# Performance work log

Measured on AMD Instinct MI355X. Metric: run time of the kernel, lower is better.

The kernel has to match this reference:

```python
import jax, jax.numpy as jnp
import numpy as np

ALPHA = 5.0
LAMBDA = 1.0


def setup_inputs() -> dict:
    key = jax.random.key(0)
    k1, k2 = jax.random.split(key)
    N, BITS, NCLASS = 2048, 64, 32
    b = jax.random.normal(k1, (N, BITS), dtype=jnp.float32)
    y = jax.random.randint(k2, (N,), 0, NCLASS, dtype=jnp.int32)
    return {"b": b, "y": y}


def reference(b, y):
    # similarity = 0.5 * <b_i, b_j>  -> [N, N]
    sim = 0.5 * (b @ b.T)
    # affinity: same-label pairs (equivalent to onehot(y) @ onehot(y).T > 0)
    aff = y[:, None] == y[None, :]  # [N, N] bool
    N = sim.shape[0]

    def step(carry, i):
        loss_sum, cnt = carry
        pos = aff[i]            # [N] bool, positives for row i
        theta = sim[i]          # [N]
        # triple[p, n] = theta_pos[p] - theta_neg[n] - alpha, clamped
        t = jnp.clip(theta[:, None] - theta[None, :] - ALPHA, -100.0, 50.0)
        # -(t - log(1 + exp(t))) == log1p(exp(t)) - t  (== softplus(-t))
        val = jnp.log1p(jnp.exp(t)) - t
        mask = pos[:, None] & (~pos)[None, :]
        npairs = mask.sum()
        valid = pos.any() & (~pos).any()
        row_loss = jnp.where(
            valid,
            jnp.where(mask, val, 0.0).sum() / jnp.maximum(npairs, 1).astype(val.dtype),
            0.0,
        )
        return (loss_sum + row_loss, cnt + valid.astype(jnp.float32)), None

    init = (jnp.float32(0.0), jnp.float32(0.0))
    (loss_sum, cnt), _ = jax.lax.scan(step, init, jnp.arange(N))
    loss1 = jnp.where(cnt > 0, loss_sum / jnp.maximum(cnt, 1.0), 0.0)
    # quantization loss (sign has zero gradient, same as torch)
    loss2 = jnp.mean((b - jnp.sign(b)) ** 2)
    total = loss1 + LAMBDA * loss2
    return total, loss1, loss2
```

## Files before the change

kernel.cpp:

```cpp
#include <hip/hip_runtime.h>
#include <math.h>

#define NROW 2048
#define BITS 64
#define MB 1024
#define RPB 8
#define JQ 2
#define NBLK (NROW / RPB)
#define NWV (MB / 64)
#define MAXPOS 256
#define MAXP2 (MAXPOS / 2)

#define LN2_F   0.6931471805599453f
#define THSCALE 0.7213475204444817f
#define A_SC    7.213475204444817f

__global__ __launch_bounds__(256) void bt_kernel(const float* __restrict__ b,
                                                 float* __restrict__ bT)
{
    __shared__ float tile[64][65];
    const int t  = threadIdx.x;
    const int j0 = blockIdx.x * 64;
    {
        const int jj = t >> 2, q = t & 3;
        const float4* b4 = reinterpret_cast<const float4*>(b + (size_t)(j0 + jj) * BITS);
#pragma unroll
        for (int m = 0; m < 4; ++m) {
            const float4 v = b4[q * 4 + m];
            const int col = q * 16 + m * 4;
            tile[jj][col + 0] = v.x; tile[jj][col + 1] = v.y;
            tile[jj][col + 2] = v.z; tile[jj][col + 3] = v.w;
        }
    }
    __syncthreads();
    {
        const int k = t >> 2, q = t & 3;
#pragma unroll
        for (int s = 0; s < 4; ++s) {
            float4 v;
            v.x = tile[q * 16 + s * 4 + 0][k];
            v.y = tile[q * 16 + s * 4 + 1][k];
            v.z = tile[q * 16 + s * 4 + 2][k];
            v.w = tile[q * 16 + s * 4 + 3][k];
            *reinterpret_cast<float4*>(&bT[(size_t)k * NROW + j0 + q * 16 + s * 4]) = v;
        }
    }
}

template <bool TR>
__global__ __launch_bounds__(MB) void dhn_main(
    const float* __restrict__ b, const float* __restrict__ bT,
    const int* __restrict__ y,
    float* __restrict__ blockLoss, float* __restrict__ blockValid,
    float* __restrict__ blockQ)
{
    const int br  = blockIdx.x;
    const int i0  = br * RPB;
    const int tid = threadIdx.x;
    const int w = tid >> 6, lane = tid & 63;

    __shared__ __align__(16) float  biT[BITS * RPB];
    __shared__ __align__(16) float  posPe[RPB][MAXPOS + 8];
    __shared__ __align__(16) float2 posSM[RPB][MAXP2 + 4];
    __shared__ int   waveTot[RPB][NWV];
    __shared__ int   waveBase[RPB][NWV];
    __shared__ int   pcnt[RPB];
    __shared__ float wred[NWV], wq[NWV];

    if (tid < BITS * RPB) {
        const int k = tid >> 3, r = tid & 7;
        biT[tid] = b[(size_t)(i0 + r) * BITS + k];
    }
    __syncthreads();

    float th[JQ][RPB] = {};
    if constexpr (TR) {
        const float2* bt2 = reinterpret_cast<const float2*>(bT);
        const float4* bi4 = reinterpret_cast<const float4*>(biT);
#pragma unroll 8
        for (int k = 0; k < BITS; ++k) {
            const float2 bj = bt2[k * (NROW / 2) + tid];
            const float4 bA = bi4[k * 2 + 0];
            const float4 bB = bi4[k * 2 + 1];
            th[0][0] += bj.x * bA.x; th[0][1] += bj.x * bA.y;
            th[0][2] += bj.x * bA.z; th[0][3] += bj.x * bA.w;
            th[0][4] += bj.x * bB.x; th[0][5] += bj.x * bB.y;
            th[0][6] += bj.x * bB.z; th[0][7] += bj.x * bB.w;
            th[1][0] += bj.y * bA.x; th[1][1] += bj.y * bA.y;
            th[1][2] += bj.y * bA.z; th[1][3] += bj.y * bA.w;
            th[1][4] += bj.y * bB.x; th[1][5] += bj.y * bB.y;
            th[1][6] += bj.y * bB.z; th[1][7] += bj.y * bB.w;
        }
    } else {
        for (int k = 0; k < BITS; ++k) {
#pragma unroll
            for (int q = 0; q < JQ; ++q) {
                const float v = b[(size_t)(JQ * tid + q) * BITS + k];
#pragma unroll
                for (int r = 0; r < RPB; ++r) th[q][r] += v * biT[k * RPB + r];
            }
        }
    }

    const int2 y2 = reinterpret_cast<const int2*>(y)[tid];
    const int yj[JQ] = { y2.x, y2.y };
    int yr[RPB];
#pragma unroll
    for (int r = 0; r < RPB; ++r) yr[r] = y[i0 + r];

    float ev[JQ][RPB];
    int pm[RPB], cnt[RPB];
#pragma unroll
    for (int r = 0; r < RPB; ++r) {
        int m = 0;
#pragma unroll
        for (int q = 0; q < JQ; ++q) {
            const float t2 = th[q][r] * THSCALE;
            const bool f = (yj[q] == yr[r]);
            ev[q][r] = __builtin_amdgcn_exp2f(f ? -t2 : t2 + A_SC);
            if (f) m |= 1 << q;
        }
        pm[r] = m;
        cnt[r] = __popc(m);
    }

    int excl[RPB];
#pragma unroll
    for (int r = 0; r < RPB; ++r) {
        int v = cnt[r];
#pragma unroll
        for (int off = 1; off < 64; off <<= 1) {
            const int t2 = __shfl_up(v, off);
            if (lane >= off) v += t2;
        }
        excl[r] = v - cnt[r];
        if (lane == 63) waveTot[r][w] = v;
    }
    __syncthreads();
    if (tid < RPB) {
        int base = 0;
#pragma unroll
        for (int wv = 0; wv < NWV; ++wv) { waveBase[tid][wv] = base; base += waveTot[tid][wv]; }
        pcnt[tid] = base;
    }
    __syncthreads();

#pragma unroll
    for (int r = 0; r < RPB; ++r) {
        int o = waveBase[r][w] + excl[r];
#pragma unroll
        for (int q = 0; q < JQ; ++q) {
            if ((pm[r] >> q) & 1) {
                if (o < MAXPOS) posPe[r][o] = ev[q][r];
                ++o;
            }
        }
    }
    if (tid < RPB * 8) {
        const int r = tid >> 3, q = tid & 7;
        const int P = pcnt[r] < MAXPOS ? pcnt[r] : MAXPOS;
        const int idx = P + q;
        if (idx < ((P + 7) & ~7)) posPe[r][idx] = 0.f;
    }
    __syncthreads();

    {
        const int r  = tid >> 7;
        const int pp = tid & 127;
        const int P  = pcnt[r] < MAXPOS ? pcnt[r] : MAXPOS;
        const int P2pad = ((P + 7) & ~7) >> 1;
        if (pp < P2pad) {
            const float p0 = posPe[r][2 * pp + 0];
            const float p1 = posPe[r][2 * pp + 1];
            posSM[r][pp] = make_float2(p0 + p1, p0 * p1);
        }
    }
    __syncthreads();

    float total = 0.f;
#pragma unroll
    for (int r = 0; r < RPB; ++r) {
        const int Pc = pcnt[r];
        const int P  = Pc < MAXPOS ? Pc : MAXPOS;
        const int PG = (((P + 7) & ~7) >> 1) >> 2;
        const float e0  = (pm[r] & 1) ? 0.f : ev[0][r];
        const float e1  = (pm[r] & 2) ? 0.f : ev[1][r];
        const float e20 = e0 * e0;
        const float e21 = e1 * e1;
        float a0 = 0.f, a1 = 0.f;
        const float4* sm4 = reinterpret_cast<const float4*>(&posSM[r][0]);
        for (int g = 0; g < PG; ++g) {
            const float4 A = sm4[2 * g + 0];
            const float4 B = sm4[2 * g + 1];
            a0 += __builtin_amdgcn_logf(fmaf(e20, A.y, fmaf(e0, A.x, 1.f)))
                + __builtin_amdgcn_logf(fmaf(e20, A.w, fmaf(e0, A.z, 1.f)))
                + __builtin_amdgcn_logf(fmaf(e20, B.y, fmaf(e0, B.x, 1.f)))
                + __builtin_amdgcn_logf(fmaf(e20, B.w, fmaf(e0, B.z, 1.f)));
            a1 += __builtin_amdgcn_logf(fmaf(e21, A.y, fmaf(e1, A.x, 1.f)))
                + __builtin_amdgcn_logf(fmaf(e21, A.w, fmaf(e1, A.z, 1.f)))
                + __builtin_amdgcn_logf(fmaf(e21, B.y, fmaf(e1, B.x, 1.f)))
                + __builtin_amdgcn_logf(fmaf(e21, B.w, fmaf(e1, B.z, 1.f)));
        }
        const bool valid = (Pc > 0) && (Pc < NROW);
        const float denom = (float)Pc * (float)(NROW - Pc);
        total += valid ? (a0 + a1) / denom : 0.f;
    }
    total *= LN2_F;

    float q2 = 0.f;
    if (tid < BITS * RPB) {
        const float x  = biT[tid];
        const float sg = (x > 0.f) ? 1.f : ((x < 0.f) ? -1.f : 0.f);
        const float d  = x - sg;
        q2 = d * d;
    }

#pragma unroll
    for (int off = 32; off > 0; off >>= 1) {
        total += __shfl_xor(total, off);
        q2    += __shfl_xor(q2, off);
    }
    if (lane == 0) { wred[w] = total; wq[w] = q2; }
    __syncthreads();
    if (tid == 0) {
        float tl = 0.f, tq = 0.f;
#pragma unroll
        for (int v = 0; v < NWV; ++v) { tl += wred[v]; tq += wq[v]; }
        blockLoss[br] = tl;
        blockQ[br]    = tq;
        float vc = 0.f;
#pragma unroll
        for (int r = 0; r < RPB; ++r)
            vc += ((pcnt[r] > 0) && (pcnt[r] < NROW)) ? 1.f : 0.f;
        blockValid[br] = vc;
    }
}

__global__ __launch_bounds__(256) void dhn_final_kernel(
    const float* __restrict__ blockLoss, const float* __restrict__ blockValid,
    const float* __restrict__ blockQ, float* __restrict__ out)
{
    const int tid = threadIdx.x;
    const int w = tid >> 6, lane = tid & 63;
    __shared__ float r1[4], r2[4], r3[4];

    float sl = 0.f, sv = 0.f, sq = 0.f;
    for (int i = tid; i < NBLK; i += 256) {
        sl += blockLoss[i]; sv += blockValid[i]; sq += blockQ[i];
    }
#pragma unroll
    for (int off = 32; off > 0; off >>= 1) {
        sl += __shfl_xor(sl, off);
        sv += __shfl_xor(sv, off);
        sq += __shfl_xor(sq, off);
    }
    if (lane == 0) { r1[w] = sl; r2[w] = sv; r3[w] = sq; }
    __syncthreads();
    if (tid == 0) {
        float SL = 0.f, SV = 0.f, SQ = 0.f;
#pragma unroll
        for (int v = 0; v < 4; ++v) { SL += r1[v]; SV += r2[v]; SQ += r3[v]; }
        const float loss1 = (SV > 0.f) ? SL / fmaxf(SV, 1.f) : 0.f;
        const float loss2 = SQ / (float)(NROW * BITS);
        out[0] = loss1 + 1.0f * loss2;
        out[1] = loss1;
        out[2] = loss2;
    }
}

extern "C" void kernel_launch(void* const* d_in, const int* in_sizes, int n_in,
                              void* d_out, int out_size, void* d_ws, size_t ws_size,
                              hipStream_t stream) {
    const float* b = (const float*)d_in[0];
    const int*   y = (const int*)d_in[1];
    float* out = (float*)d_out;

    float* blockLoss  = (float*)d_ws;
    float* blockValid = (float*)((char*)d_ws + 4096);
    float* blockQ     = (float*)((char*)d_ws + 8192);
    float* bT         = (float*)((char*)d_ws + 16384);

    const size_t need = 16384 + (size_t)BITS * NROW * sizeof(float);
    if (ws_size >= need) {
        bt_kernel<<<NROW / 64, 256, 0, stream>>>(b, bT);
        dhn_main<true><<<NBLK, MB, 0, stream>>>(b, bT, y, blockLoss, blockValid, blockQ);
    } else {
        dhn_main<false><<<NBLK, MB, 0, stream>>>(b, nullptr, y, blockLoss, blockValid, blockQ);
    }
    dhn_final_kernel<<<1, 256, 0, stream>>>(blockLoss, blockValid, blockQ, out);
}
```

Baseline: 45.90 us.

## Precompute positives by label bucketing and split columns across two blocks

Adds a prep kernel that builds a per-label histogram and an index list, plus a pos kernel that computes each row's positive exp terms directly from that list. The main kernel no longer needs block-wide prefix scans and compaction, and runs over a 2D grid so each 512-thread block handles half of the columns. The aim is to remove the heavy scan and sync phases and to raise parallelism. In exchange it adds two extra launches and global round trips, drops the fallback path when the workspace is too small, and lowers the positive cap to 128.

```diff
diff --git a/kernel.cpp b/kernel.cpp
--- a/kernel.cpp
+++ b/kernel.cpp
@@ -3,83 +3,152 @@
 
 #define NROW 2048
 #define BITS 64
-#define MB 1024
+#define MB 512
 #define RPB 8
 #define JQ 2
-#define NBLK (NROW / RPB)
-#define NWV (MB / 64)
-#define MAXPOS 256
-#define MAXP2 (MAXPOS / 2)
+#define NRG (NROW / RPB)
+#define NSL 2
+#define JSL (NROW / NSL)
+#define MAXPOS 128
 
 #define LN2_F   0.6931471805599453f
 #define THSCALE 0.7213475204444817f
 #define A_SC    7.213475204444817f
 
-__global__ __launch_bounds__(256) void bt_kernel(const float* __restrict__ b,
-                                                 float* __restrict__ bT)
-{
-    __shared__ float tile[64][65];
-    const int t  = threadIdx.x;
-    const int j0 = blockIdx.x * 64;
-    {
-        const int jj = t >> 2, q = t & 3;
-        const float4* b4 = reinterpret_cast<const float4*>(b + (size_t)(j0 + jj) * BITS);
-#pragma unroll
-        for (int m = 0; m < 4; ++m) {
-            const float4 v = b4[q * 4 + m];
-            const int col = q * 16 + m * 4;
-            tile[jj][col + 0] = v.x; tile[jj][col + 1] = v.y;
-            tile[jj][col + 2] = v.z; tile[jj][col + 3] = v.w;
-        }
-    }
-    __syncthreads();
-    {
-        const int k = t >> 2, q = t & 3;
-#pragma unroll
-        for (int s = 0; s < 4; ++s) {
-            float4 v;
-            v.x = tile[q * 16 + s * 4 + 0][k];
-            v.y = tile[q * 16 + s * 4 + 1][k];
-            v.z = tile[q * 16 + s * 4 + 2][k];
-            v.w = tile[q * 16 + s * 4 + 3][k];
-            *reinterpret_cast<float4*>(&bT[(size_t)k * NROW + j0 + q * 16 + s * 4]) = v;
-        }
-    }
-}
-
-template <bool TR>
+__global__ __launch_bounds__(256) void prep_kernel(
+    const float* __restrict__ b, const int* __restrict__ y,
+    float* __restrict__ bT, int* __restrict__ offG, int* __restrict__ idxG)
+{
+    union U {
+        float tile[64][65];
+        struct { int ys[NROW]; int hist[32]; int offL[33]; } s;
+    };
+    __shared__ U u;
+    const int t = threadIdx.x;
+
+    if (blockIdx.x < 32) {
+        const int j0 = blockIdx.x * 64;
+        {
+            const int jj = t >> 2, q = t & 3;
+            const float4* b4 = reinterpret_cast<const float4*>(b + (size_t)(j0 + jj) * BITS);
+#pragma unroll
+            for (int m = 0; m < 4; ++m) {
+                const float4 v = b4[q * 4 + m];
+                const int col = q * 16 + m * 4;
+                u.tile[jj][col + 0] = v.x; u.tile[jj][col + 1] = v.y;
+                u.tile[jj][col + 2] = v.z; u.tile[jj][col + 3] = v.w;
+            }
+        }
+        __syncthreads();
+        {
+            const int k = t >> 2, q = t & 3;
+#pragma unroll
+            for (int s = 0; s < 4; ++s) {
+                float4 v;
+                v.x = u.tile[q * 16 + s * 4 + 0][k];
+                v.y = u.tile[q * 16 + s * 4 + 1][k];
+                v.z = u.tile[q * 16 + s * 4 + 2][k];
+                v.w = u.tile[q * 16 + s * 4 + 3][k];
+                *reinterpret_cast<float4*>(&bT[(size_t)k * NROW + j0 + q * 16 + s * 4]) = v;
+            }
+        }
+        return;
+    }
+
+    for (int k = t; k < NROW; k += 256) u.s.ys[k] = y[k];
+    if (t < 32) u.s.hist[t] = 0;
+    __syncthreads();
+    for (int k = t; k < NROW; k += 256) atomicAdd(&u.s.hist[u.s.ys[k]], 1);
+    __syncthreads();
+    const int w = t >> 6, lane = t & 63;
+    if (w == 0) {
+        int v = (lane < 32) ? u.s.hist[lane] : 0;
+#pragma unroll
+        for (int off = 1; off < 32; off <<= 1) {
+            const int tv = __shfl_up(v, off);
+            if (lane >= off) v += tv;
+        }
+        if (lane < 32) { u.s.offL[lane + 1] = v; offG[lane + 1] = v; }
+        if (lane == 0) { u.s.offL[0] = 0; offG[0] = 0; }
+    }
+    __syncthreads();
+    const unsigned long long lm = (1ull << lane) - 1ull;
+    for (int s8 = 0; s8 < 8; ++s8) {
+        const int lab = w * 8 + s8;
+        int base = u.s.offL[lab];
+        for (int c = 0; c < NROW / 64; ++c) {
+            const int j = c * 64 + lane;
+            const bool f = (u.s.ys[j] == lab);
+            const unsigned long long mp = __ballot(f);
+            if (f) idxG[base + (int)__popcll(mp & lm)] = j;
+            base += (int)__popcll(mp);
+        }
+    }
+}
+
+__global__ __launch_bounds__(256) void pos_kernel(
+    const float* __restrict__ b, const int* __restrict__ y,
+    const int* __restrict__ offG, const int* __restrict__ idxG,
+    float* __restrict__ posPeG)
+{
+    __shared__ __align__(16) float biS[4][BITS];
+    const int t = threadIdx.x, w = t >> 6, lane = t & 63;
+    const int i = blockIdx.x * 4 + w;
+    if (lane < BITS) biS[w][lane] = b[(size_t)i * BITS + lane];
+    __syncthreads();
+    const int yi = y[i];
+    const int st = offG[yi];
+    const int P  = offG[yi + 1] - st;
+    const float4* bi4 = reinterpret_cast<const float4*>(&biS[w][0]);
+    for (int p = lane; p < MAXPOS; p += 64) {
+        float val = 0.f;
+        if (p < P) {
+            const int jp = idxG[st + p];
+            const float4* rp = reinterpret_cast<const float4*>(b + (size_t)jp * BITS);
+            float acc = 0.f;
+#pragma unroll
+            for (int k4 = 0; k4 < BITS / 4; ++k4) {
+                const float4 a = bi4[k4], v = rp[k4];
+                acc += a.x * v.x + a.y * v.y + a.z * v.z + a.w * v.w;
+            }
+            val = __builtin_amdgcn_exp2f(-THSCALE * acc);
+        }
+        posPeG[(size_t)i * MAXPOS + p] = val;
+    }
+}
+
 __global__ __launch_bounds__(MB) void dhn_main(
     const float* __restrict__ b, const float* __restrict__ bT,
-    const int* __restrict__ y,
-    float* __restrict__ blockLoss, float* __restrict__ blockValid,
-    float* __restrict__ blockQ)
-{
-    const int br  = blockIdx.x;
-    const int i0  = br * RPB;
-    const int tid = threadIdx.x;
+    const int* __restrict__ y, const int* __restrict__ offG,
+    const float* __restrict__ posPeG,
+    float* __restrict__ blockLoss, float* __restrict__ blockQ)
+{
+    const int rg    = blockIdx.x;
+    const int slice = blockIdx.y;
+    const int i0    = rg * RPB;
+    const int tid   = threadIdx.x;
     const int w = tid >> 6, lane = tid & 63;
 
     __shared__ __align__(16) float  biT[BITS * RPB];
-    __shared__ __align__(16) float  posPe[RPB][MAXPOS + 8];
-    __shared__ __align__(16) float2 posSM[RPB][MAXP2 + 4];
-    __shared__ int   waveTot[RPB][NWV];
-    __shared__ int   waveBase[RPB][NWV];
-    __shared__ int   pcnt[RPB];
-    __shared__ float wred[NWV], wq[NWV];
-
-    if (tid < BITS * RPB) {
-        const int k = tid >> 3, r = tid & 7;
-        biT[tid] = b[(size_t)(i0 + r) * BITS + k];
+    __shared__ __align__(16) float2 posSM[RPB][MAXPOS / 2];
+    __shared__ float wred[MB / 64], wq[MB / 64];
+
+    biT[tid] = b[(size_t)(i0 + (tid & 7)) * BITS + (tid >> 3)];
+    {
+        const float2 pg = reinterpret_cast<const float2*>(posPeG)
+                              [(size_t)(i0 + w) * (MAXPOS / 2) + lane];
+        posSM[w][lane] = make_float2(pg.x + pg.y, pg.x * pg.y);
     }
     __syncthreads();
 
     float th[JQ][RPB] = {};
-    if constexpr (TR) {
+    {
         const float2* bt2 = reinterpret_cast<const float2*>(bT);
         const float4* bi4 = reinterpret_cast<const float4*>(biT);
+        const int jb = slice * (JSL / 2) + tid;
 #pragma unroll 8
         for (int k = 0; k < BITS; ++k) {
-            const float2 bj = bt2[k * (NROW / 2) + tid];
+            const float2 bj = bt2[k * (NROW / 2) + jb];
             const float4 bA = bi4[k * 2 + 0];
             const float4 bB = bi4[k * 2 + 1];
             th[0][0] += bj.x * bA.x; th[0][1] += bj.x * bA.y;
@@ -91,124 +160,43 @@
             th[1][4] += bj.y * bB.x; th[1][5] += bj.y * bB.y;
             th[1][6] += bj.y * bB.z; th[1][7] += bj.y * bB.w;
         }
-    } else {
-        for (int k = 0; k < BITS; ++k) {
-#pragma unroll
-            for (int q = 0; q < JQ; ++q) {
-                const float v = b[(size_t)(JQ * tid + q) * BITS + k];
-#pragma unroll
-                for (int r = 0; r < RPB; ++r) th[q][r] += v * biT[k * RPB + r];
-            }
-        }
-    }
-
-    const int2 y2 = reinterpret_cast<const int2*>(y)[tid];
-    const int yj[JQ] = { y2.x, y2.y };
-    int yr[RPB];
-#pragma unroll
-    for (int r = 0; r < RPB; ++r) yr[r] = y[i0 + r];
-
-    float ev[JQ][RPB];
-    int pm[RPB], cnt[RPB];
+    }
+    const int2 y2 = reinterpret_cast<const int2*>(y)[slice * (JSL / 2) + tid];
+
+    float total = 0.f;
 #pragma unroll
     for (int r = 0; r < RPB; ++r) {
-        int m = 0;
-#pragma unroll
-        for (int q = 0; q < JQ; ++q) {
-            const float t2 = th[q][r] * THSCALE;
-            const bool f = (yj[q] == yr[r]);
-            ev[q][r] = __builtin_amdgcn_exp2f(f ? -t2 : t2 + A_SC);
-            if (f) m |= 1 << q;
-        }
-        pm[r] = m;
-        cnt[r] = __popc(m);
-    }
-
-    int excl[RPB];
-#pragma unroll
-    for (int r = 0; r < RPB; ++r) {
-        int v = cnt[r];
-#pragma unroll
-        for (int off = 1; off < 64; off <<= 1) {
-            const int t2 = __shfl_up(v, off);
-            if (lane >= off) v += t2;
-        }
-        excl[r] = v - cnt[r];
-        if (lane == 63) waveTot[r][w] = v;
-    }
-    __syncthreads();
-    if (tid < RPB) {
-        int base = 0;
-#pragma unroll
-        for (int wv = 0; wv < NWV; ++wv) { waveBase[tid][wv] = base; base += waveTot[tid][wv]; }
-        pcnt[tid] = base;
-    }
-    __syncthreads();
-
-#pragma unroll
-    for (int r = 0; r < RPB; ++r) {
-        int o = waveBase[r][w] + excl[r];
-#pragma unroll
-        for (int q = 0; q < JQ; ++q) {
-            if ((pm[r] >> q) & 1) {
-                if (o < MAXPOS) posPe[r][o] = ev[q][r];
-                ++o;
-            }
-        }
-    }
-    if (tid < RPB * 8) {
-        const int r = tid >> 3, q = tid & 7;
-        const int P = pcnt[r] < MAXPOS ? pcnt[r] : MAXPOS;
-        const int idx = P + q;
-        if (idx < ((P + 7) & ~7)) posPe[r][idx] = 0.f;
-    }
-    __syncthreads();
-
-    {
-        const int r  = tid >> 7;
-        const int pp = tid & 127;
-        const int P  = pcnt[r] < MAXPOS ? pcnt[r] : MAXPOS;
-        const int P2pad = ((P + 7) & ~7) >> 1;
-        if (pp < P2pad) {
-            const float p0 = posPe[r][2 * pp + 0];
-            const float p1 = posPe[r][2 * pp + 1];
-            posSM[r][pp] = make_float2(p0 + p1, p0 * p1);
-        }
-    }
-    __syncthreads();
-
-    float total = 0.f;
-#pragma unroll
-    for (int r = 0; r < RPB; ++r) {
-        const int Pc = pcnt[r];
-        const int P  = Pc < MAXPOS ? Pc : MAXPOS;
-        const int PG = (((P + 7) & ~7) >> 1) >> 2;
-        const float e0  = (pm[r] & 1) ? 0.f : ev[0][r];
-        const float e1  = (pm[r] & 2) ? 0.f : ev[1][r];
-        const float e20 = e0 * e0;
-        const float e21 = e1 * e1;
-        float a0 = 0.f, a1 = 0.f;
+        const int yr = y[i0 + r];
+        const int P  = offG[yr + 1] - offG[yr];
+        const int PG = ((P + 7) & ~7) >> 3;
+        const float x0 = __builtin_amdgcn_exp2f(th[0][r] * THSCALE + A_SC);
+        const float x1 = __builtin_amdgcn_exp2f(th[1][r] * THSCALE + A_SC);
+        const float e0 = (y2.x == yr) ? 0.f : x0;
+        const float e1 = (y2.y == yr) ? 0.f : x1;
+        const float e20 = e0 * e0, e21 = e1 * e1;
+        float la0 = 0.f, la1 = 0.f;
         const float4* sm4 = reinterpret_cast<const float4*>(&posSM[r][0]);
         for (int g = 0; g < PG; ++g) {
             const float4 A = sm4[2 * g + 0];
             const float4 B = sm4[2 * g + 1];
-            a0 += __builtin_amdgcn_logf(fmaf(e20, A.y, fmaf(e0, A.x, 1.f)))
-                + __builtin_amdgcn_logf(fmaf(e20, A.w, fmaf(e0, A.z, 1.f)))
-                + __builtin_amdgcn_logf(fmaf(e20, B.y, fmaf(e0, B.x, 1.f)))
-                + __builtin_amdgcn_logf(fmaf(e20, B.w, fmaf(e0, B.z, 1.f)));
-            a1 += __builtin_amdgcn_logf(fmaf(e21, A.y, fmaf(e1, A.x, 1.f)))
-                + __builtin_amdgcn_logf(fmaf(e21, A.w, fmaf(e1, A.z, 1.f)))
-                + __builtin_amdgcn_logf(fmaf(e21, B.y, fmaf(e1, B.x, 1.f)))
-                + __builtin_amdgcn_logf(fmaf(e21, B.w, fmaf(e1, B.z, 1.f)));
-        }
-        const bool valid = (Pc > 0) && (Pc < NROW);
-        const float denom = (float)Pc * (float)(NROW - Pc);
-        total += valid ? (a0 + a1) / denom : 0.f;
+            la0 += (__builtin_amdgcn_logf(fmaf(e20, A.y, fmaf(e0, A.x, 1.f)))
+                  + __builtin_amdgcn_logf(fmaf(e20, A.w, fmaf(e0, A.z, 1.f))))
+                 + (__builtin_amdgcn_logf(fmaf(e20, B.y, fmaf(e0, B.x, 1.f)))
+                  + __builtin_amdgcn_logf(fmaf(e20, B.w, fmaf(e0, B.z, 1.f))));
+            la1 += (__builtin_amdgcn_logf(fmaf(e21, A.y, fmaf(e1, A.x, 1.f)))
+                  + __builtin_amdgcn_logf(fmaf(e21, A.w, fmaf(e1, A.z, 1.f))))
+                 + (__builtin_amdgcn_logf(fmaf(e21, B.y, fmaf(e1, B.x, 1.f)))
+                  + __builtin_amdgcn_logf(fmaf(e21, B.w, fmaf(e1, B.z, 1.f))));
+        }
+        if (P < NROW) {
+            const float denom = (float)P * (float)(NROW - P);
+            total += (la0 + la1) / denom;
+        }
     }
     total *= LN2_F;
 
     float q2 = 0.f;
-    if (tid < BITS * RPB) {
+    if (slice == 0) {
         const float x  = biT[tid];
         const float sg = (x > 0.f) ? 1.f : ((x < 0.f) ? -1.f : 0.f);
         const float d  = x - sg;
@@ -225,28 +213,28 @@
     if (tid == 0) {
         float tl = 0.f, tq = 0.f;
 #pragma unroll
-        for (int v = 0; v < NWV; ++v) { tl += wred[v]; tq += wq[v]; }
-        blockLoss[br] = tl;
-        blockQ[br]    = tq;
-        float vc = 0.f;
-#pragma unroll
-        for (int r = 0; r < RPB; ++r)
-            vc += ((pcnt[r] > 0) && (pcnt[r] < NROW)) ? 1.f : 0.f;
-        blockValid[br] = vc;
+        for (int v = 0; v < MB / 64; ++v) { tl += wred[v]; tq += wq[v]; }
+        blockLoss[slice * NRG + rg] = tl;
+        if (slice == 0) blockQ[rg] = tq;
     }
 }
 
 __global__ __launch_bounds__(256) void dhn_final_kernel(
-    const float* __restrict__ blockLoss, const float* __restrict__ blockValid,
-    const float* __restrict__ blockQ, float* __restrict__ out)
+    const int* __restrict__ y, const int* __restrict__ offG,
+    const float* __restrict__ blockLoss, const float* __restrict__ blockQ,
+    float* __restrict__ out)
 {
     const int tid = threadIdx.x;
     const int w = tid >> 6, lane = tid & 63;
     __shared__ float r1[4], r2[4], r3[4];
 
     float sl = 0.f, sv = 0.f, sq = 0.f;
-    for (int i = tid; i < NBLK; i += 256) {
-        sl += blockLoss[i]; sv += blockValid[i]; sq += blockQ[i];
+    for (int i = tid; i < NSL * NRG; i += 256) sl += blockLoss[i];
+    for (int i = tid; i < NRG; i += 256) sq += blockQ[i];
+    for (int i = tid; i < NROW; i += 256) {
+        const int yi = y[i];
+        const int P = offG[yi + 1] - offG[yi];
+        sv += ((P > 0) && (P < NROW)) ? 1.f : 0.f;
     }
 #pragma unroll
     for (int off = 32; off > 0; off >>= 1) {
@@ -275,17 +263,16 @@
     const int*   y = (const int*)d_in[1];
     float* out = (float*)d_out;
 
-    float* blockLoss  = (float*)d_ws;
-    float* blockValid = (float*)((char*)d_ws + 4096);
-    float* blockQ     = (float*)((char*)d_ws + 8192);
-    float* bT         = (float*)((char*)d_ws + 16384);
-
-    const size_t need = 16384 + (size_t)BITS * NROW * sizeof(float);
-    if (ws_size >= need) {
-        bt_kernel<<<NROW / 64, 256, 0, stream>>>(b, bT);
-        dhn_main<true><<<NBLK, MB, 0, stream>>>(b, bT, y, blockLoss, blockValid, blockQ);
-    } else {
-        dhn_main<false><<<NBLK, MB, 0, stream>>>(b, nullptr, y, blockLoss, blockValid, blockQ);
-    }
-    dhn_final_kernel<<<1, 256, 0, stream>>>(blockLoss, blockValid, blockQ, out);
-}
+    int*   offG      = (int*)d_ws;
+    int*   idxG      = (int*)((char*)d_ws + 1024);
+    float* blockLoss = (float*)((char*)d_ws + 10240);
+    float* blockQ    = (float*)((char*)d_ws + 12800);
+    float* posPeG    = (float*)((char*)d_ws + 16384);
+    float* bT        = (float*)((char*)d_ws + 16384 + 1048576);
+
+    prep_kernel<<<33, 256, 0, stream>>>(b, y, bT, offG, idxG);
+    pos_kernel<<<NROW / 4, 256, 0, stream>>>(b, y, offG, idxG, posPeG);
+    dhn_main<<<dim3(NRG, NSL), MB, 0, stream>>>(b, bT, y, offG, posPeG,
+                                                blockLoss, blockQ);
+    dhn_final_kernel<<<1, 256, 0, stream>>>(y, offG, blockLoss, blockQ, out);
+}
```

Result: slower. 60.03 us (+30.8%).
